# Kernel optimization log

Measured on AMD Instinct MI355X. Metric: run time of the kernel, lower is better.

## Reference

```python
import jax, jax.numpy as jnp
import numpy as np

B, N, IN_F, OUT_F, H = 4, 2048, 256, 64, 8


def setup_inputs() -> dict:
    key = jax.random.key(0)
    k1, k2, k3, k4, k5 = jax.random.split(key, 5)
    x = jax.random.normal(k1, (B, N, IN_F), dtype=jnp.float32)
    adj = jax.random.randint(k2, (B, N, N), 0, 2, dtype=jnp.int32)
    # xavier-uniform-ish scaled params
    w_lim = float(np.sqrt(6.0 / (IN_F + H * OUT_F)))
    a_lim = float(np.sqrt(6.0 / (OUT_F + 1)))
    weight = jax.random.uniform(k3, (IN_F, H * OUT_F), minval=-w_lim, maxval=w_lim, dtype=jnp.float32)
    attn_src = jax.random.uniform(k4, (H, OUT_F), minval=-a_lim, maxval=a_lim, dtype=jnp.float32)
    attn_dst = jax.random.uniform(k5, (H, OUT_F), minval=-a_lim, maxval=a_lim, dtype=jnp.float32)
    return {"x": x, "adj": adj, "weight": weight, "attn_src": attn_src, "attn_dst": attn_dst}


def reference(x, adj, weight, attn_src, attn_dst):
    b, n, _ = x.shape
    # linear projection -> per-head features  [B,N,H,F]
    h = jnp.matmul(x, weight).reshape(b, n, H, OUT_F)
    # additive attention logits
    src = jnp.einsum('bnhf,hf->bnh', h, attn_src)  # [B,N,H]
    dst = jnp.einsum('bnhf,hf->bnh', h, attn_dst)  # [B,N,H]
    # scores[b,i,j,h] = src[b,i,h] + dst[b,j,h]   -> [B,N,N,H]
    scores = src[:, :, None, :] + dst[:, None, :, :]
    mask = (adj == 0)[..., None]  # [B,N,N,1]
    scores = jnp.where(mask, -jnp.inf, scores)
    attn = jax.nn.softmax(scores, axis=2)  # softmax over neighbors j
    # aggregation (intended math of the torch matmul): [B,N,H,F]
    h_prime = jnp.einsum('bijh,bjhf->bihf', attn, h)
    # concat heads
    return h_prime.reshape(b, n, H * OUT_F)
```

## Files before the change

kernel.cpp:

```cpp
#include <hip/hip_runtime.h>
#include <hip/hip_bf16.h>
#include <math.h>

#define B_    4
#define N_    2048
#define INF_  256
#define OUTF_ 64
#define H_    8
#define C_    512

typedef __attribute__((ext_vector_type(8))) short  bf16x8;
typedef __attribute__((ext_vector_type(4))) short  s16x4;
typedef __attribute__((ext_vector_type(4))) float  f32x4;

static __device__ __forceinline__ short f2b(float f) {
    union { float f; unsigned u; } v; v.f = f;
    unsigned r = (v.u + 0x7FFFu + ((v.u >> 16) & 1u)) >> 16;
    return (short)r;
}
static __device__ __forceinline__ float b2f(short s) {
    union { unsigned u; float f; } v; v.u = ((unsigned)(unsigned short)s) << 16;
    return v.f;
}
static __device__ __forceinline__ unsigned long long mk64(int lo, int hi) {
    return ((unsigned long long)(unsigned)hi << 32) | (unsigned)lo;
}

#define GL2LDS(gsrc, ldst)                                                          \
    __builtin_amdgcn_global_load_lds(                                               \
        (const __attribute__((address_space(1))) void*)(gsrc),                      \
        (__attribute__((address_space(3))) void*)(ldst), 16, 0, 0)

#define WAITV2() asm volatile("s_waitcnt vmcnt(2)" ::: "memory")
#define WAITV0() asm volatile("s_waitcnt vmcnt(0)" ::: "memory")
#define WAITLG() asm volatile("s_waitcnt lgkmcnt(0)" ::: "memory")
#define BAR()    do { asm volatile("" ::: "memory"); __builtin_amdgcn_s_barrier(); \
                      asm volatile("" ::: "memory"); } while (0)

__global__ __launch_bounds__(256)
void cast_xw(const float* __restrict__ x, const float* __restrict__ w,
             short* __restrict__ xb, short* __restrict__ wbT) {
    __shared__ short T[64][72];
    const int bid = blockIdx.x;
    if (bid < 1024) {
        size_t i8 = (size_t)bid * 256 + threadIdx.x;
        const float4* p = reinterpret_cast<const float4*>(x + i8 * 8);
        float4 v0 = p[0], v1 = p[1];
        bf16x8 o;
        o[0] = f2b(v0.x); o[1] = f2b(v0.y); o[2] = f2b(v0.z); o[3] = f2b(v0.w);
        o[4] = f2b(v1.x); o[5] = f2b(v1.y); o[6] = f2b(v1.z); o[7] = f2b(v1.w);
        *reinterpret_cast<bf16x8*>(xb + i8 * 8) = o;
    } else {
        int blk = bid - 1024;
        int c0 = (blk & 7) * 64;
        int k0 = (blk >> 3) * 64;
        int t = threadIdx.x;
        int cl = (t & 15) * 4;
#pragma unroll
        for (int p = 0; p < 4; ++p) {
            int kl = p * 16 + (t >> 4);
            float4 v = *reinterpret_cast<const float4*>(&w[(size_t)(k0 + kl) * C_ + c0 + cl]);
            T[cl + 0][kl] = f2b(v.x);
            T[cl + 1][kl] = f2b(v.y);
            T[cl + 2][kl] = f2b(v.z);
            T[cl + 3][kl] = f2b(v.w);
        }
        __syncthreads();
        int cr = t >> 2;
        int ks = (t & 3) * 16;
        short* dst = &wbT[(size_t)(c0 + cr) * INF_ + k0 + ks];
        *reinterpret_cast<bf16x8*>(dst)     = *reinterpret_cast<const bf16x8*>(&T[cr][ks]);
        *reinterpret_cast<bf16x8*>(dst + 8) = *reinterpret_cast<const bf16x8*>(&T[cr][ks + 8]);
    }
}

__global__ __launch_bounds__(256)
void proj_pack(const short* __restrict__ xb, const short* __restrict__ wbT,
               const float* __restrict__ attn_dst, const int* __restrict__ adj,
               short* __restrict__ ebT, short* __restrict__ gT,
               unsigned char* __restrict__ bm) {
    __shared__ char smem[24576];
    const int sub = blockIdx.x >> 1;
    if (blockIdx.x & 1) {
        const int wid  = threadIdx.x >> 6;
        const int lane = threadIdx.x & 63;
        const int rowbase = sub * 16 + wid * 4;
#pragma unroll
        for (int rr = 0; rr < 4; ++rr) {
            const int row = rowbase + rr;
            const int* arow = adj + (size_t)row * N_;
            unsigned long long myword = 0;
#pragma unroll
            for (int it = 0; it < 32; ++it) {
                unsigned long long m = __ballot(arow[it * 64 + lane] != 0);
                if (lane == it) myword = m;
            }
            if (lane < 32)
                *reinterpret_cast<unsigned long long*>(bm + (size_t)row * 256 + lane * 8) = myword;
        }
        return;
    }
    short* As = (short*)smem;
    short* Bs = (short*)(smem + 16384);
    short* Tt = (short*)smem;
    float* Sr = (float*)(smem + 17408);
    short* Eb = (short*)(smem + 18432);

    const int m0 = (sub & 63) * 128;
    const int n0 = (sub >> 6) * 64;
    const int head = n0 >> 6;
    const int b    = m0 >> 11;
    const int j0g  = m0 & (N_ - 1);
    const int wid  = threadIdx.x >> 6;
    const int lane = threadIdx.x & 63;
    const int wr = wid >> 1, wc = wid & 1;
    const int q4 = lane >> 4, l15 = lane & 15;
    const int lr = lane >> 3;
    const int ls = (lane & 7) ^ lr;
    const short* Abase = xb + (size_t)m0 * INF_;
    const short* Bbase = wbT + (size_t)n0 * INF_;

    f32x4 acc[4][2];
#pragma unroll
    for (int m = 0; m < 4; ++m)
#pragma unroll
        for (int n = 0; n < 2; ++n) acc[m][n] = (f32x4){0.f, 0.f, 0.f, 0.f};

    for (int k0 = 0; k0 < INF_; k0 += 64) {
#pragma unroll
        for (int q = 0; q < 4; ++q) {
            int chunk = wid * 4 + q;
            int row   = chunk * 8 + lr;
            GL2LDS(Abase + (size_t)row * INF_ + k0 + ls * 8, As + chunk * 512);
        }
#pragma unroll
        for (int q = 0; q < 2; ++q) {
            int chunk = wid * 2 + q;
            int row   = chunk * 8 + lr;
            GL2LDS(Bbase + (size_t)row * INF_ + k0 + ls * 8, Bs + chunk * 512);
        }
        __syncthreads();
#pragma unroll
        for (int kk = 0; kk < 2; ++kk) {
            const int ko = kk * 32 + q4 * 8;
            bf16x8 a[4], bb[2];
#pragma unroll
            for (int m = 0; m < 4; ++m) {
                int row = wr * 64 + m * 16 + l15;
                a[m] = *reinterpret_cast<const bf16x8*>(&As[row * 64 + (ko ^ ((row & 7) * 8))]);
            }
#pragma unroll
            for (int n = 0; n < 2; ++n) {
                int row = wc * 32 + n * 16 + l15;
                bb[n] = *reinterpret_cast<const bf16x8*>(&Bs[row * 64 + (ko ^ ((row & 7) * 8))]);
            }
#pragma unroll
            for (int m = 0; m < 4; ++m)
#pragma unroll
                for (int n = 0; n < 2; ++n)
                    acc[m][n] = __builtin_amdgcn_mfma_f32_16x16x32_bf16(a[m], bb[n], acc[m][n], 0, 0, 0);
        }
        __syncthreads();
    }

    float af0 = attn_dst[head * 64 + wc * 32 + l15];
    float af1 = attn_dst[head * 64 + wc * 32 + 16 + l15];
#pragma unroll
    for (int m = 0; m < 4; ++m) {
        f32x4 part;
#pragma unroll
        for (int r = 0; r < 4; ++r)
            part[r] = acc[m][0][r] * af0 + acc[m][1][r] * af1;
#pragma unroll
        for (int off = 1; off < 16; off <<= 1)
#pragma unroll
            for (int r = 0; r < 4; ++r) part[r] += __shfl_xor(part[r], off);
        if (l15 == 0)
            *reinterpret_cast<f32x4*>(&Sr[wc * 128 + wr * 64 + m * 16 + q4 * 4]) = part;
    }
    __syncthreads();
    const int t = threadIdx.x;
    if (t < 128) {
        float s = Sr[t] + Sr[128 + t];
        short eb = f2b(expf(s));
        Eb[t] = eb;
        ebT[((size_t)b * H_ + head) * N_ + j0g + t] = eb;
    }
    __syncthreads();
#pragma unroll
    for (int m = 0; m < 4; ++m) {
        int jl = wr * 64 + m * 16 + q4 * 4;
        float ev[4];
#pragma unroll
        for (int r = 0; r < 4; ++r) ev[r] = b2f(Eb[jl + r]);
#pragma unroll
        for (int n = 0; n < 2; ++n) {
            int cl = wc * 32 + n * 16 + l15;
            s16x4 gv;
#pragma unroll
            for (int r = 0; r < 4; ++r) gv[r] = f2b(acc[m][n][r] * ev[r]);
            *reinterpret_cast<s16x4*>(&Tt[cl * 136 + jl]) = gv;
        }
    }
    __syncthreads();
    {
        int c  = t >> 2;
        int jc = (t & 3) * 32;
        short* dst = &gT[((size_t)b * C_ + n0 + c) * N_ + j0g + jc];
#pragma unroll
        for (int u = 0; u < 4; ++u)
            *reinterpret_cast<bf16x8*>(dst + u * 8) =
                *reinterpret_cast<const bf16x8*>(&Tt[c * 136 + jc + u * 8]);
    }
}

__global__ __launch_bounds__(512, 4)
void agg_mfma(const unsigned char* __restrict__ bm, const short* __restrict__ gT,
              const short* __restrict__ ebT, float* __restrict__ out) {
    __shared__ short Bs[6][4096];
    __shared__ short Es[2048];
    __shared__ float Dr[128];
    __shared__ short LUT[64];

    const int work = (blockIdx.x & 7) * 64 + (blockIdx.x >> 3);
    const int mt = work & 15;
    const int nt = (work >> 4) & 7;
    const int b  = work >> 7;
    const int m0 = mt * 128;
    const int n0 = nt * 64;

    const int tid  = threadIdx.x;
    const int wid  = tid >> 6;
    const int lane = tid & 63;
    const int wr = wid >> 1, wc = wid & 1;
    const int q4 = lane >> 4, l15 = lane & 15;
    const int lr = lane >> 3;
    const int ls = (lane & 7) ^ lr;

    if (tid < 64)
        LUT[tid] = ((((tid >> 2)) >> (tid & 3)) & 1) ? (short)0x3F80 : (short)0;

    const short* Bbase = gT + ((size_t)b * C_ + n0) * N_;
    const unsigned char* M0 = bm + ((size_t)b * N_ + m0 + wr * 32 + l15) * 256;
    const unsigned char* M1 = M0 + 16 * 256;

#define STAGE1(buf, k0s) \
    GL2LDS(Bbase + (size_t)(wid * 8 + lr) * N_ + (k0s) + ls * 8, (buf) + wid * 512)

#define EXPAND(byte_) ({                                                             \
        union { bf16x8 v_; unsigned long long q_[2]; } u_;                           \
        u_.q_[0] = *reinterpret_cast<const unsigned long long*>(&LUT[((byte_) & 15u) * 4]); \
        u_.q_[1] = *reinterpret_cast<const unsigned long long*>(&LUT[(((byte_) >> 4) & 15u) * 4]); \
        u_.v_; })

    f32x4 acc[2][2];
    f32x4 accd = (f32x4){0.f, 0.f, 0.f, 0.f};
#pragma unroll
    for (int m = 0; m < 2; ++m)
#pragma unroll
        for (int n = 0; n < 2; ++n) acc[m][n] = (f32x4){0.f, 0.f, 0.f, 0.f};

#define COMPUTE_T(bufp, k0_, abits0, abits1) do {                                    \
        _Pragma("unroll")                                                            \
        for (int kk = 0; kk < 2; ++kk) {                                             \
            const int gA = kk * 4 + q4;                                              \
            bf16x8 a0 = EXPAND((unsigned)((abits0) >> (gA * 8)) & 0xFFu);            \
            bf16x8 a1 = EXPAND((unsigned)((abits1) >> (gA * 8)) & 0xFFu);            \
            bf16x8 b0, b1, be;                                                       \
            { int row = wc * 32 + l15;                                               \
              b0 = *reinterpret_cast<const bf16x8*>(&(bufp)[row * 64 + ((gA ^ (row & 7)) * 8)]); } \
            { int row = wc * 32 + 16 + l15;                                          \
              b1 = *reinterpret_cast<const bf16x8*>(&(bufp)[row * 64 + ((gA ^ (row & 7)) * 8)]); } \
            be = *reinterpret_cast<const bf16x8*>(&Es[(k0_) + gA * 8]);              \
            acc[0][0] = __builtin_amdgcn_mfma_f32_16x16x32_bf16(a0, b0, acc[0][0], 0, 0, 0); \
            acc[0][1] = __builtin_amdgcn_mfma_f32_16x16x32_bf16(a0, b1, acc[0][1], 0, 0, 0); \
            acc[1][0] = __builtin_amdgcn_mfma_f32_16x16x32_bf16(a1, b0, acc[1][0], 0, 0, 0); \
            acc[1][1] = __builtin_amdgcn_mfma_f32_16x16x32_bf16(a1, b1, acc[1][1], 0, 0, 0); \
            accd = __builtin_amdgcn_mfma_f32_16x16x32_bf16(wc ? a1 : a0, be, accd, 0, 0, 0); \
        }                                                                            \
    } while (0)

    int4 a0c = *reinterpret_cast<const int4*>(M0);
    int4 a1c = *reinterpret_cast<const int4*>(M1);
    if (wid < 4)
        GL2LDS(ebT + ((size_t)b * H_ + nt) * N_ + wid * 512 + lane * 8, Es + wid * 512);
    short *cA = &Bs[0][0], *cB = &Bs[1][0];
    short *nA = &Bs[2][0], *nB = &Bs[3][0];
    short *sA = &Bs[4][0], *sB = &Bs[5][0];
    STAGE1(cA, 0);
    STAGE1(cB, 64);
    STAGE1(nA, 128);
    STAGE1(nB, 192);
    WAITLG();
    WAITV0();
    BAR();

    int4 a0n, a1n;
    for (int p = 0; p < 14; ++p) {
        a0n = *reinterpret_cast<const int4*>(M0 + (p + 1) * 16);
        a1n = *reinterpret_cast<const int4*>(M1 + (p + 1) * 16);
        STAGE1(sA, p * 128 + 256);
        STAGE1(sB, p * 128 + 320);
        COMPUTE_T(cA, p * 128,      mk64(a0c.x, a0c.y), mk64(a1c.x, a1c.y));
        COMPUTE_T(cB, p * 128 + 64, mk64(a0c.z, a0c.w), mk64(a1c.z, a1c.w));
        WAITV2();
        BAR();
        short* t0 = cA; short* t1 = cB;
        cA = nA; cB = nB; nA = sA; nB = sB; sA = t0; sB = t1;
        a0c = a0n; a1c = a1n;
    }
    a0n = *reinterpret_cast<const int4*>(M0 + 15 * 16);
    a1n = *reinterpret_cast<const int4*>(M1 + 15 * 16);
    COMPUTE_T(cA, 14 * 128,      mk64(a0c.x, a0c.y), mk64(a1c.x, a1c.y));
    COMPUTE_T(cB, 14 * 128 + 64, mk64(a0c.z, a0c.w), mk64(a1c.z, a1c.w));
    WAITV0();
    BAR();
    cA = nA; cB = nB; a0c = a0n; a1c = a1n;
    COMPUTE_T(cA, 15 * 128,      mk64(a0c.x, a0c.y), mk64(a1c.x, a1c.y));
    COMPUTE_T(cB, 15 * 128 + 64, mk64(a0c.z, a0c.w), mk64(a1c.z, a1c.w));

    if (l15 == 0)
        *reinterpret_cast<f32x4*>(&Dr[wr * 32 + wc * 16 + q4 * 4]) = accd;
    __syncthreads();

    float* obase = out + ((size_t)b * N_ + m0) * C_ + n0;
#pragma unroll
    for (int m = 0; m < 2; ++m) {
        int rbase = wr * 32 + m * 16 + q4 * 4;
        float inv[4];
#pragma unroll
        for (int r = 0; r < 4; ++r) inv[r] = 1.0f / Dr[rbase + r];
#pragma unroll
        for (int n = 0; n < 2; ++n) {
            int gc = wc * 32 + n * 16 + l15;
#pragma unroll
            for (int r = 0; r < 4; ++r)
                obase[(size_t)(rbase + r) * C_ + gc] = acc[m][n][r] * inv[r];
        }
    }
#undef STAGE1
#undef COMPUTE_T
#undef EXPAND
}

extern "C" void kernel_launch(void* const* d_in, const int* in_sizes, int n_in,
                              void* d_out, int out_size, void* d_ws, size_t ws_size,
                              hipStream_t stream) {
    const float* x        = (const float*)d_in[0];
    const int*   adj      = (const int*)d_in[1];
    const float* weight   = (const float*)d_in[2];
    const float* attn_dst = (const float*)d_in[4];
    float* out = (float*)d_out;

    short* xb  = (short*)d_ws;
    short* wbT = xb + (size_t)B_ * N_ * INF_;
    short* ebT = wbT + (size_t)C_ * INF_;
    short* gT  = ebT + (size_t)B_ * H_ * N_;
    unsigned char* bmp = (unsigned char*)(gT + (size_t)B_ * C_ * N_);

    cast_xw<<<dim3(1024 + 32), 256, 0, stream>>>(x, weight, xb, wbT);
    proj_pack<<<dim3(1024), 256, 0, stream>>>(xb, wbT, attn_dst, adj, ebT, gT, bmp);
    agg_mfma<<<dim3(512), 512, 0, stream>>>(bmp, gT, ebT, out);
}
```

Before: 50.80 us.

## Widen aggregation tile to two heads per block and expand mask bits in registers

The aggregation kernel now computes a 128x128 output tile (two heads) per block instead of 128x64, so each expanded adjacency-bit A fragment feeds twice as many MFMAs and the bitmap is read half as often. Each wave keeps its own denominator accumulators, which removes the shared Dr buffer and a barrier. The LDS lookup table for bit expansion is replaced with in-register select logic. In exchange LDS use and register pressure roughly double, occupancy drops (launch bound 2 instead of 4), and the grid shrinks to 256 blocks, which may underfill the GPU's compute units.

```diff
diff --git a/kernel.cpp b/kernel.cpp
--- a/kernel.cpp
+++ b/kernel.cpp
@@ -25,15 +25,20 @@
 static __device__ __forceinline__ unsigned long long mk64(int lo, int hi) {
     return ((unsigned long long)(unsigned)hi << 32) | (unsigned)lo;
 }
+static __device__ __forceinline__ bf16x8 bits2bf16(unsigned byte) {
+    bf16x8 f;
+#pragma unroll
+    for (int u = 0; u < 8; ++u) f[u] = ((byte >> u) & 1u) ? (short)0x3F80 : (short)0;
+    return f;
+}
 
 #define GL2LDS(gsrc, ldst)                                                          \
     __builtin_amdgcn_global_load_lds(                                               \
         (const __attribute__((address_space(1))) void*)(gsrc),                      \
         (__attribute__((address_space(3))) void*)(ldst), 16, 0, 0)
 
-#define WAITV2() asm volatile("s_waitcnt vmcnt(2)" ::: "memory")
+#define WAITV4() asm volatile("s_waitcnt vmcnt(4)" ::: "memory")
 #define WAITV0() asm volatile("s_waitcnt vmcnt(0)" ::: "memory")
-#define WAITLG() asm volatile("s_waitcnt lgkmcnt(0)" ::: "memory")
 #define BAR()    do { asm volatile("" ::: "memory"); __builtin_amdgcn_s_barrier(); \
                       asm volatile("" ::: "memory"); } while (0)
 
@@ -214,20 +219,19 @@
     }
 }
 
-__global__ __launch_bounds__(512, 4)
+__global__ __launch_bounds__(512, 2)
 void agg_mfma(const unsigned char* __restrict__ bm, const short* __restrict__ gT,
               const short* __restrict__ ebT, float* __restrict__ out) {
-    __shared__ short Bs[6][4096];
-    __shared__ short Es[2048];
-    __shared__ float Dr[128];
-    __shared__ short LUT[64];
-
-    const int work = (blockIdx.x & 7) * 64 + (blockIdx.x >> 3);
+    __shared__ short Bs[6][8192];
+    __shared__ short Es[2][2048];
+
+    const int work = (blockIdx.x & 7) * 32 + (blockIdx.x >> 3);
     const int mt = work & 15;
-    const int nt = (work >> 4) & 7;
-    const int b  = work >> 7;
+    const int nt = (work >> 4) & 3;
+    const int b  = work >> 6;
     const int m0 = mt * 128;
-    const int n0 = nt * 64;
+    const int n0 = nt * 128;
+    const int h0 = n0 >> 6;
 
     const int tid  = threadIdx.x;
     const int wid  = tid >> 6;
@@ -237,61 +241,61 @@
     const int lr = lane >> 3;
     const int ls = (lane & 7) ^ lr;
 
-    if (tid < 64)
-        LUT[tid] = ((((tid >> 2)) >> (tid & 3)) & 1) ? (short)0x3F80 : (short)0;
-
     const short* Bbase = gT + ((size_t)b * C_ + n0) * N_;
     const unsigned char* M0 = bm + ((size_t)b * N_ + m0 + wr * 32 + l15) * 256;
     const unsigned char* M1 = M0 + 16 * 256;
 
-#define STAGE1(buf, k0s) \
-    GL2LDS(Bbase + (size_t)(wid * 8 + lr) * N_ + (k0s) + ls * 8, (buf) + wid * 512)
-
-#define EXPAND(byte_) ({                                                             \
-        union { bf16x8 v_; unsigned long long q_[2]; } u_;                           \
-        u_.q_[0] = *reinterpret_cast<const unsigned long long*>(&LUT[((byte_) & 15u) * 4]); \
-        u_.q_[1] = *reinterpret_cast<const unsigned long long*>(&LUT[(((byte_) >> 4) & 15u) * 4]); \
-        u_.v_; })
-
-    f32x4 acc[2][2];
-    f32x4 accd = (f32x4){0.f, 0.f, 0.f, 0.f};
-#pragma unroll
-    for (int m = 0; m < 2; ++m)
-#pragma unroll
-        for (int n = 0; n < 2; ++n) acc[m][n] = (f32x4){0.f, 0.f, 0.f, 0.f};
+#define STAGE_T(buf, k0s) do {                                                       \
+        GL2LDS(Bbase + (size_t)(wid * 16 + lr) * N_ + (k0s) + ls * 8,                \
+               (buf) + wid * 1024);                                                  \
+        GL2LDS(Bbase + (size_t)(wid * 16 + 8 + lr) * N_ + (k0s) + ls * 8,            \
+               (buf) + wid * 1024 + 512);                                            \
+    } while (0)
+
+    f32x4 acc[2][4];
+    f32x4 accd[2];
+#pragma unroll
+    for (int m = 0; m < 2; ++m) {
+        accd[m] = (f32x4){0.f, 0.f, 0.f, 0.f};
+#pragma unroll
+        for (int n = 0; n < 4; ++n) acc[m][n] = (f32x4){0.f, 0.f, 0.f, 0.f};
+    }
 
 #define COMPUTE_T(bufp, k0_, abits0, abits1) do {                                    \
         _Pragma("unroll")                                                            \
         for (int kk = 0; kk < 2; ++kk) {                                             \
             const int gA = kk * 4 + q4;                                              \
-            bf16x8 a0 = EXPAND((unsigned)((abits0) >> (gA * 8)) & 0xFFu);            \
-            bf16x8 a1 = EXPAND((unsigned)((abits1) >> (gA * 8)) & 0xFFu);            \
-            bf16x8 b0, b1, be;                                                       \
-            { int row = wc * 32 + l15;                                               \
-              b0 = *reinterpret_cast<const bf16x8*>(&(bufp)[row * 64 + ((gA ^ (row & 7)) * 8)]); } \
-            { int row = wc * 32 + 16 + l15;                                          \
-              b1 = *reinterpret_cast<const bf16x8*>(&(bufp)[row * 64 + ((gA ^ (row & 7)) * 8)]); } \
-            be = *reinterpret_cast<const bf16x8*>(&Es[(k0_) + gA * 8]);              \
-            acc[0][0] = __builtin_amdgcn_mfma_f32_16x16x32_bf16(a0, b0, acc[0][0], 0, 0, 0); \
-            acc[0][1] = __builtin_amdgcn_mfma_f32_16x16x32_bf16(a0, b1, acc[0][1], 0, 0, 0); \
-            acc[1][0] = __builtin_amdgcn_mfma_f32_16x16x32_bf16(a1, b0, acc[1][0], 0, 0, 0); \
-            acc[1][1] = __builtin_amdgcn_mfma_f32_16x16x32_bf16(a1, b1, acc[1][1], 0, 0, 0); \
-            accd = __builtin_amdgcn_mfma_f32_16x16x32_bf16(wc ? a1 : a0, be, accd, 0, 0, 0); \
+            bf16x8 a0 = bits2bf16((unsigned)((abits0) >> (gA * 8)) & 0xFFu);         \
+            bf16x8 a1 = bits2bf16((unsigned)((abits1) >> (gA * 8)) & 0xFFu);         \
+            bf16x8 bb[4];                                                            \
+            _Pragma("unroll")                                                        \
+            for (int n = 0; n < 4; ++n) {                                            \
+                int row = wc * 64 + n * 16 + l15;                                    \
+                bb[n] = *reinterpret_cast<const bf16x8*>(                            \
+                    &(bufp)[row * 64 + ((gA ^ (row & 7)) * 8)]);                     \
+            }                                                                        \
+            bf16x8 be = *reinterpret_cast<const bf16x8*>(&Es[wc][(k0_) + gA * 8]);   \
+            _Pragma("unroll")                                                        \
+            for (int n = 0; n < 4; ++n) {                                            \
+                acc[0][n] = __builtin_amdgcn_mfma_f32_16x16x32_bf16(a0, bb[n], acc[0][n], 0, 0, 0); \
+                acc[1][n] = __builtin_amdgcn_mfma_f32_16x16x32_bf16(a1, bb[n], acc[1][n], 0, 0, 0); \
+            }                                                                        \
+            accd[0] = __builtin_amdgcn_mfma_f32_16x16x32_bf16(a0, be, accd[0], 0, 0, 0); \
+            accd[1] = __builtin_amdgcn_mfma_f32_16x16x32_bf16(a1, be, accd[1], 0, 0, 0); \
         }                                                                            \
     } while (0)
 
     int4 a0c = *reinterpret_cast<const int4*>(M0);
     int4 a1c = *reinterpret_cast<const int4*>(M1);
-    if (wid < 4)
-        GL2LDS(ebT + ((size_t)b * H_ + nt) * N_ + wid * 512 + lane * 8, Es + wid * 512);
+    GL2LDS(ebT + ((size_t)b * H_ + h0 + (wid >> 2)) * N_ + (wid & 3) * 512 + lane * 8,
+           (short*)Es + wid * 512);
     short *cA = &Bs[0][0], *cB = &Bs[1][0];
     short *nA = &Bs[2][0], *nB = &Bs[3][0];
     short *sA = &Bs[4][0], *sB = &Bs[5][0];
-    STAGE1(cA, 0);
-    STAGE1(cB, 64);
-    STAGE1(nA, 128);
-    STAGE1(nB, 192);
-    WAITLG();
+    STAGE_T(cA, 0);
+    STAGE_T(cB, 64);
+    STAGE_T(nA, 128);
+    STAGE_T(nB, 192);
     WAITV0();
     BAR();
 
@@ -299,11 +303,11 @@
     for (int p = 0; p < 14; ++p) {
         a0n = *reinterpret_cast<const int4*>(M0 + (p + 1) * 16);
         a1n = *reinterpret_cast<const int4*>(M1 + (p + 1) * 16);
-        STAGE1(sA, p * 128 + 256);
-        STAGE1(sB, p * 128 + 320);
+        STAGE_T(sA, p * 128 + 256);
+        STAGE_T(sB, p * 128 + 320);
         COMPUTE_T(cA, p * 128,      mk64(a0c.x, a0c.y), mk64(a1c.x, a1c.y));
         COMPUTE_T(cB, p * 128 + 64, mk64(a0c.z, a0c.w), mk64(a1c.z, a1c.w));
-        WAITV2();
+        WAITV4();
         BAR();
         short* t0 = cA; short* t1 = cB;
         cA = nA; cB = nB; nA = sA; nB = sB; sA = t0; sB = t1;
@@ -319,28 +323,23 @@
     COMPUTE_T(cA, 15 * 128,      mk64(a0c.x, a0c.y), mk64(a1c.x, a1c.y));
     COMPUTE_T(cB, 15 * 128 + 64, mk64(a0c.z, a0c.w), mk64(a1c.z, a1c.w));
 
-    if (l15 == 0)
-        *reinterpret_cast<f32x4*>(&Dr[wr * 32 + wc * 16 + q4 * 4]) = accd;
-    __syncthreads();
-
-    float* obase = out + ((size_t)b * N_ + m0) * C_ + n0;
+    float* obase = out + ((size_t)b * N_ + m0) * C_ + n0 + wc * 64;
 #pragma unroll
     for (int m = 0; m < 2; ++m) {
         int rbase = wr * 32 + m * 16 + q4 * 4;
         float inv[4];
 #pragma unroll
-        for (int r = 0; r < 4; ++r) inv[r] = 1.0f / Dr[rbase + r];
-#pragma unroll
-        for (int n = 0; n < 2; ++n) {
-            int gc = wc * 32 + n * 16 + l15;
+        for (int r = 0; r < 4; ++r) inv[r] = 1.0f / accd[m][r];
+#pragma unroll
+        for (int n = 0; n < 4; ++n) {
+            int gc = n * 16 + l15;
 #pragma unroll
             for (int r = 0; r < 4; ++r)
                 obase[(size_t)(rbase + r) * C_ + gc] = acc[m][n][r] * inv[r];
         }
     }
-#undef STAGE1
+#undef STAGE_T
 #undef COMPUTE_T
-#undef EXPAND
 }
 
 extern "C" void kernel_launch(void* const* d_in, const int* in_sizes, int n_in,
@@ -360,5 +359,5 @@
 
     cast_xw<<<dim3(1024 + 32), 256, 0, stream>>>(x, weight, xb, wbT);
     proj_pack<<<dim3(1024), 256, 0, stream>>>(xb, wbT, attn_dst, adj, ebT, gT, bmp);
-    agg_mfma<<<dim3(512), 512, 0, stream>>>(bmp, gT, ebT, out);
-}
+    agg_mfma<<<dim3(256), 512, 0, stream>>>(bmp, gT, ebT, out);
+}
```

Result: slower. 56.86 us (+11.9%).

## Halve aggregation block to 256 threads with larger per-wave 64x32 tiles

Applied to the files above, without the earlier changes.

The aggregation kernel now runs 4 waves per block instead of 8, and each wave computes a 64-row by 32-column tile (four A fragments) instead of 32x32. Each B fragment read from LDS is reused across twice as many MFMAs, and the denominator MFMA is split into two accumulators. Staging issues two global-to-LDS loads per wave and the wait count is raised to match. More accumulator registers per thread and fewer waves per block may reduce latency hiding.

```diff
diff --git a/kernel.cpp b/kernel.cpp
--- a/kernel.cpp
+++ b/kernel.cpp
@@ -31,7 +31,7 @@
         (const __attribute__((address_space(1))) void*)(gsrc),                      \
         (__attribute__((address_space(3))) void*)(ldst), 16, 0, 0)
 
-#define WAITV2() asm volatile("s_waitcnt vmcnt(2)" ::: "memory")
+#define WAITV4() asm volatile("s_waitcnt vmcnt(4)" ::: "memory")
 #define WAITV0() asm volatile("s_waitcnt vmcnt(0)" ::: "memory")
 #define WAITLG() asm volatile("s_waitcnt lgkmcnt(0)" ::: "memory")
 #define BAR()    do { asm volatile("" ::: "memory"); __builtin_amdgcn_s_barrier(); \
@@ -214,7 +214,7 @@
     }
 }
 
-__global__ __launch_bounds__(512, 4)
+__global__ __launch_bounds__(256, 2)
 void agg_mfma(const unsigned char* __restrict__ bm, const short* __restrict__ gT,
               const short* __restrict__ ebT, float* __restrict__ out) {
     __shared__ short Bs[6][4096];
@@ -241,11 +241,14 @@
         LUT[tid] = ((((tid >> 2)) >> (tid & 3)) & 1) ? (short)0x3F80 : (short)0;
 
     const short* Bbase = gT + ((size_t)b * C_ + n0) * N_;
-    const unsigned char* M0 = bm + ((size_t)b * N_ + m0 + wr * 32 + l15) * 256;
-    const unsigned char* M1 = M0 + 16 * 256;
-
-#define STAGE1(buf, k0s) \
-    GL2LDS(Bbase + (size_t)(wid * 8 + lr) * N_ + (k0s) + ls * 8, (buf) + wid * 512)
+    const unsigned char* Mb = bm + ((size_t)b * N_ + m0 + wr * 64 + l15) * 256;
+
+#define STAGE_T(buf, k0s) do {                                                       \
+        GL2LDS(Bbase + (size_t)(wid * 16 + lr) * N_ + (k0s) + ls * 8,                \
+               (buf) + wid * 1024);                                                  \
+        GL2LDS(Bbase + (size_t)(wid * 16 + 8 + lr) * N_ + (k0s) + ls * 8,            \
+               (buf) + wid * 1024 + 512);                                            \
+    } while (0)
 
 #define EXPAND(byte_) ({                                                             \
         union { bf16x8 v_; unsigned long long q_[2]; } u_;                           \
@@ -253,19 +256,23 @@
         u_.q_[1] = *reinterpret_cast<const unsigned long long*>(&LUT[(((byte_) >> 4) & 15u) * 4]); \
         u_.v_; })
 
-    f32x4 acc[2][2];
-    f32x4 accd = (f32x4){0.f, 0.f, 0.f, 0.f};
-#pragma unroll
-    for (int m = 0; m < 2; ++m)
+    f32x4 acc[4][2];
+    f32x4 accd[2];
+#pragma unroll
+    for (int m = 0; m < 4; ++m)
 #pragma unroll
         for (int n = 0; n < 2; ++n) acc[m][n] = (f32x4){0.f, 0.f, 0.f, 0.f};
-
-#define COMPUTE_T(bufp, k0_, abits0, abits1) do {                                    \
+    accd[0] = (f32x4){0.f, 0.f, 0.f, 0.f};
+    accd[1] = (f32x4){0.f, 0.f, 0.f, 0.f};
+
+#define COMPUTE_T(bufp, k0_, u0_, u1_, u2_, u3_) do {                                \
         _Pragma("unroll")                                                            \
         for (int kk = 0; kk < 2; ++kk) {                                             \
             const int gA = kk * 4 + q4;                                              \
-            bf16x8 a0 = EXPAND((unsigned)((abits0) >> (gA * 8)) & 0xFFu);            \
-            bf16x8 a1 = EXPAND((unsigned)((abits1) >> (gA * 8)) & 0xFFu);            \
+            bf16x8 a0 = EXPAND((unsigned)((u0_) >> (gA * 8)) & 0xFFu);               \
+            bf16x8 a1 = EXPAND((unsigned)((u1_) >> (gA * 8)) & 0xFFu);               \
+            bf16x8 a2 = EXPAND((unsigned)((u2_) >> (gA * 8)) & 0xFFu);               \
+            bf16x8 a3 = EXPAND((unsigned)((u3_) >> (gA * 8)) & 0xFFu);               \
             bf16x8 b0, b1, be;                                                       \
             { int row = wc * 32 + l15;                                               \
               b0 = *reinterpret_cast<const bf16x8*>(&(bufp)[row * 64 + ((gA ^ (row & 7)) * 8)]); } \
@@ -276,57 +283,75 @@
             acc[0][1] = __builtin_amdgcn_mfma_f32_16x16x32_bf16(a0, b1, acc[0][1], 0, 0, 0); \
             acc[1][0] = __builtin_amdgcn_mfma_f32_16x16x32_bf16(a1, b0, acc[1][0], 0, 0, 0); \
             acc[1][1] = __builtin_amdgcn_mfma_f32_16x16x32_bf16(a1, b1, acc[1][1], 0, 0, 0); \
-            accd = __builtin_amdgcn_mfma_f32_16x16x32_bf16(wc ? a1 : a0, be, accd, 0, 0, 0); \
+            acc[2][0] = __builtin_amdgcn_mfma_f32_16x16x32_bf16(a2, b0, acc[2][0], 0, 0, 0); \
+            acc[2][1] = __builtin_amdgcn_mfma_f32_16x16x32_bf16(a2, b1, acc[2][1], 0, 0, 0); \
+            acc[3][0] = __builtin_amdgcn_mfma_f32_16x16x32_bf16(a3, b0, acc[3][0], 0, 0, 0); \
+            acc[3][1] = __builtin_amdgcn_mfma_f32_16x16x32_bf16(a3, b1, acc[3][1], 0, 0, 0); \
+            accd[0] = __builtin_amdgcn_mfma_f32_16x16x32_bf16(wc ? a2 : a0, be, accd[0], 0, 0, 0); \
+            accd[1] = __builtin_amdgcn_mfma_f32_16x16x32_bf16(wc ? a3 : a1, be, accd[1], 0, 0, 0); \
         }                                                                            \
     } while (0)
 
-    int4 a0c = *reinterpret_cast<const int4*>(M0);
-    int4 a1c = *reinterpret_cast<const int4*>(M1);
-    if (wid < 4)
-        GL2LDS(ebT + ((size_t)b * H_ + nt) * N_ + wid * 512 + lane * 8, Es + wid * 512);
+    int4 c0 = *reinterpret_cast<const int4*>(Mb);
+    int4 c1 = *reinterpret_cast<const int4*>(Mb + 16 * 256);
+    int4 c2 = *reinterpret_cast<const int4*>(Mb + 32 * 256);
+    int4 c3 = *reinterpret_cast<const int4*>(Mb + 48 * 256);
+    GL2LDS(ebT + ((size_t)b * H_ + nt) * N_ + wid * 512 + lane * 8, Es + wid * 512);
     short *cA = &Bs[0][0], *cB = &Bs[1][0];
     short *nA = &Bs[2][0], *nB = &Bs[3][0];
     short *sA = &Bs[4][0], *sB = &Bs[5][0];
-    STAGE1(cA, 0);
-    STAGE1(cB, 64);
-    STAGE1(nA, 128);
-    STAGE1(nB, 192);
+    STAGE_T(cA, 0);
+    STAGE_T(cB, 64);
+    STAGE_T(nA, 128);
+    STAGE_T(nB, 192);
     WAITLG();
-    WAITV0();
+    WAITV4();
     BAR();
 
-    int4 a0n, a1n;
+    int4 n0c, n1c, n2c, n3c;
     for (int p = 0; p < 14; ++p) {
-        a0n = *reinterpret_cast<const int4*>(M0 + (p + 1) * 16);
-        a1n = *reinterpret_cast<const int4*>(M1 + (p + 1) * 16);
-        STAGE1(sA, p * 128 + 256);
-        STAGE1(sB, p * 128 + 320);
-        COMPUTE_T(cA, p * 128,      mk64(a0c.x, a0c.y), mk64(a1c.x, a1c.y));
-        COMPUTE_T(cB, p * 128 + 64, mk64(a0c.z, a0c.w), mk64(a1c.z, a1c.w));
-        WAITV2();
+        n0c = *reinterpret_cast<const int4*>(Mb + (p + 1) * 16);
+        n1c = *reinterpret_cast<const int4*>(Mb + 16 * 256 + (p + 1) * 16);
+        n2c = *reinterpret_cast<const int4*>(Mb + 32 * 256 + (p + 1) * 16);
+        n3c = *reinterpret_cast<const int4*>(Mb + 48 * 256 + (p + 1) * 16);
+        STAGE_T(sA, p * 128 + 256);
+        STAGE_T(sB, p * 128 + 320);
+        COMPUTE_T(cA, p * 128,      mk64(c0.x, c0.y), mk64(c1.x, c1.y),
+                                    mk64(c2.x, c2.y), mk64(c3.x, c3.y));
+        COMPUTE_T(cB, p * 128 + 64, mk64(c0.z, c0.w), mk64(c1.z, c1.w),
+                                    mk64(c2.z, c2.w), mk64(c3.z, c3.w));
+        WAITV4();
         BAR();
         short* t0 = cA; short* t1 = cB;
         cA = nA; cB = nB; nA = sA; nB = sB; sA = t0; sB = t1;
-        a0c = a0n; a1c = a1n;
-    }
-    a0n = *reinterpret_cast<const int4*>(M0 + 15 * 16);
-    a1n = *reinterpret_cast<const int4*>(M1 + 15 * 16);
-    COMPUTE_T(cA, 14 * 128,      mk64(a0c.x, a0c.y), mk64(a1c.x, a1c.y));
-    COMPUTE_T(cB, 14 * 128 + 64, mk64(a0c.z, a0c.w), mk64(a1c.z, a1c.w));
+        c0 = n0c; c1 = n1c; c2 = n2c; c3 = n3c;
+    }
+    n0c = *reinterpret_cast<const int4*>(Mb + 15 * 16);
+    n1c = *reinterpret_cast<const int4*>(Mb + 16 * 256 + 15 * 16);
+    n2c = *reinterpret_cast<const int4*>(Mb + 32 * 256 + 15 * 16);
+    n3c = *reinterpret_cast<const int4*>(Mb + 48 * 256 + 15 * 16);
+    COMPUTE_T(cA, 14 * 128,      mk64(c0.x, c0.y), mk64(c1.x, c1.y),
+                                 mk64(c2.x, c2.y), mk64(c3.x, c3.y));
+    COMPUTE_T(cB, 14 * 128 + 64, mk64(c0.z, c0.w), mk64(c1.z, c1.w),
+                                 mk64(c2.z, c2.w), mk64(c3.z, c3.w));
     WAITV0();
     BAR();
-    cA = nA; cB = nB; a0c = a0n; a1c = a1n;
-    COMPUTE_T(cA, 15 * 128,      mk64(a0c.x, a0c.y), mk64(a1c.x, a1c.y));
-    COMPUTE_T(cB, 15 * 128 + 64, mk64(a0c.z, a0c.w), mk64(a1c.z, a1c.w));
-
-    if (l15 == 0)
-        *reinterpret_cast<f32x4*>(&Dr[wr * 32 + wc * 16 + q4 * 4]) = accd;
+    cA = nA; cB = nB; c0 = n0c; c1 = n1c; c2 = n2c; c3 = n3c;
+    COMPUTE_T(cA, 15 * 128,      mk64(c0.x, c0.y), mk64(c1.x, c1.y),
+                                 mk64(c2.x, c2.y), mk64(c3.x, c3.y));
+    COMPUTE_T(cB, 15 * 128 + 64, mk64(c0.z, c0.w), mk64(c1.z, c1.w),
+                                 mk64(c2.z, c2.w), mk64(c3.z, c3.w));
+
+    if (l15 == 0) {
+        *reinterpret_cast<f32x4*>(&Dr[wr * 64 + (2 * wc) * 16 + q4 * 4])     = accd[0];
+        *reinterpret_cast<f32x4*>(&Dr[wr * 64 + (2 * wc + 1) * 16 + q4 * 4]) = accd[1];
+    }
     __syncthreads();
 
     float* obase = out + ((size_t)b * N_ + m0) * C_ + n0;
 #pragma unroll
-    for (int m = 0; m < 2; ++m) {
-        int rbase = wr * 32 + m * 16 + q4 * 4;
+    for (int m = 0; m < 4; ++m) {
+        int rbase = wr * 64 + m * 16 + q4 * 4;
         float inv[4];
 #pragma unroll
         for (int r = 0; r < 4; ++r) inv[r] = 1.0f / Dr[rbase + r];
@@ -338,7 +363,7 @@
                 obase[(size_t)(rbase + r) * C_ + gc] = acc[m][n][r] * inv[r];
         }
     }
-#undef STAGE1
+#undef STAGE_T
 #undef COMPUTE_T
 #undef EXPAND
 }
@@ -360,5 +385,5 @@
 
     cast_xw<<<dim3(1024 + 32), 256, 0, stream>>>(x, weight, xb, wbT);
     proj_pack<<<dim3(1024), 256, 0, stream>>>(xb, wbT, attn_dst, adj, ebT, gT, bmp);
-    agg_mfma<<<dim3(512), 512, 0, stream>>>(bmp, gT, ebT, out);
-}
+    agg_mfma<<<dim3(512), 256, 0, stream>>>(bmp, gT, ebT, out);
+}
```

New measurement: 52.59 us. 3.5% more time.
